# Kernel tuning notes

Measured on AMD Instinct MI355X. Metric: run time of the kernel, lower is better.

Reference implementation:

```python
import jax, jax.numpy as jnp
import numpy as np

N_TASKS = 32
D = 2097152  # flattened gradient dim
MAX_ITER = 250
STOP_CRIT = 1e-6
EPS = 1e-8


def setup_inputs() -> dict:
    key = jax.random.key(0)
    vecs = jax.random.normal(key, (N_TASKS, D), dtype=jnp.float32)
    return {"vecs": vecs}


def _line_solver(v11, v12, v22):
    # min-norm point on the segment between two vectors (vectorized / scalar)
    g = (v22 - v12) / (v11 + v22 - 2.0 * v12 + EPS)
    c = v22 + g * (v12 - v22)
    gamma = jnp.where(v12 >= v22, 0.0, g)
    gamma = jnp.where(v12 >= v11, 1.0, gamma)
    cost = jnp.where(v12 >= v22, v22, c)
    cost = jnp.where(v12 >= v11, v11, cost)
    return gamma, cost


def _planar_init(G, n):
    iu_np, ju_np = np.triu_indices(n, 1)
    iu = jnp.asarray(iu_np)
    ju = jnp.asarray(ju_np)
    vivj = G[iu, ju]
    vivi = G[iu, iu]
    vjvj = G[ju, ju]
    gamma, cost = _line_solver(vivi, vivj, vjvj)
    off = jnp.argmin(cost)
    sol = jnp.zeros(n, dtype=G.dtype)
    sol = sol.at[iu[off]].set(gamma[off]).at[ju[off]].set(1.0 - gamma[off])
    return sol


def _proj_simplex(gamma, i_grid):
    s = jnp.sort(gamma)[::-1]  # descending
    tmp_max = (jnp.cumsum(s) - 1.0) / i_grid
    cond = tmp_max[:-1] > s[1:]
    first = jnp.argmax(cond)  # index of first True (0 if none)
    tmax = jnp.where(jnp.any(cond), tmp_max[:-1][first], tmp_max[-1])
    return jnp.maximum(gamma - tmax, 0.0)


def _next_point(cur, grad, n, i_grid):
    proj = grad - jnp.sum(grad) / n
    neg = proj < 0
    pos = proj > 0
    tm1 = jnp.where(neg, -cur / jnp.where(neg, proj, 1.0), jnp.inf)
    tm2 = jnp.where(pos, (1.0 - cur) / jnp.where(pos, proj, 1.0), jnp.inf)
    m1 = jnp.min(jnp.where(tm1 > 1e-7, tm1, jnp.inf))
    t = jnp.where(jnp.isfinite(m1), m1, 1.0)
    m2 = jnp.min(jnp.where(tm2 > 1e-7, tm2, jnp.inf))
    t = jnp.minimum(t, m2)  # no-op if m2 is inf
    nxt = proj * t + cur
    return _proj_simplex(nxt, i_grid)


def reference(vecs):
    n = vecs.shape[0]
    G = vecs @ vecs.T  # [n, n] grammian; only memory-heavy step
    sol0 = _planar_init(G, n)
    i_grid = jnp.arange(n, dtype=G.dtype) + 1.0
    n_f = jnp.asarray(n, dtype=G.dtype)

    def body(carry, _):
        sol, done = carry
        grad_dir = -(G @ sol)
        newp = _next_point(sol, grad_dir, n_f, i_grid)
        Gs = G @ sol
        Gn = G @ newp
        v11 = sol @ Gs
        v12 = sol @ Gn
        v22 = newp @ Gn
        gamma, _ = _line_solver(v11, v12, v22)
        new_sol = gamma * sol + (1.0 - gamma) * newp
        stop = jnp.sum(jnp.abs(new_sol - sol)) < STOP_CRIT
        nd = done | stop
        # original returns the OLD sol_vec when change < stop_crit
        out = jnp.where(nd, sol, new_sol)
        return (out, nd), None

    (sol, _), _ = jax.lax.scan(body, (sol0, jnp.array(False)), None, length=MAX_ITER)
    return sol
```

## Files before the change

### kernel.cpp

```cpp
#include <hip/hip_runtime.h>

#define NT 32
#define EPSF 1e-8f

#define TILE_COLS 64
#define GR_THREADS 256
#define WAVES_PB 4
#define TILES_PW 8

__global__ __launch_bounds__(GR_THREADS, 1)
void gram_kernel(const float* __restrict__ vecs, double* __restrict__ Gd, int D)
{
    __shared__ __align__(16) float tile[WAVES_PB][TILE_COLS * 32];
    __shared__ float Gpart[NT * NT];

    const int tid  = threadIdx.x;
    const int wave = tid >> 6;
    const int lane = tid & 63;

    for (int e = tid; e < NT * NT; e += GR_THREADS) Gpart[e] = 0.0f;
    __syncthreads();

    float* my = tile[wave];
    const int swz = lane & 7;

    const int cj = lane >> 4;
    const int pi = (lane >> 2) & 3;
    const int pk = lane & 3;

    float acc[8][8];
#pragma unroll
    for (int r = 0; r < 8; r++)
#pragma unroll
        for (int c = 0; c < 8; c++) acc[r][c] = 0.0f;

    const unsigned base0 = (unsigned)blockIdx.x * (WAVES_PB * TILES_PW * TILE_COLS)
                         + (unsigned)wave * (TILES_PW * TILE_COLS) + (unsigned)lane;

    float pre[32];
#pragma unroll
    for (int r = 0; r < 32; r++)
        pre[r] = (vecs + (size_t)r * (size_t)D)[base0];

    for (int t = 0; t < TILES_PW; t++) {
#pragma unroll
        for (int g = 0; g < 8; g++) {
            float4 w = make_float4(pre[4 * g + 0], pre[4 * g + 1],
                                   pre[4 * g + 2], pre[4 * g + 3]);
            *(float4*)(my + lane * 32 + ((g ^ swz) << 2)) = w;
        }
        if (t + 1 < TILES_PW) {
            const unsigned off = base0 + (unsigned)(t + 1) * TILE_COLS;
#pragma unroll
            for (int r = 0; r < 32; r++)
                pre[r] = (vecs + (size_t)r * (size_t)D)[off];
        }
        asm volatile("" ::: "memory");
#pragma unroll
        for (int jt = 0; jt < 16; jt++) {
            const int j = (jt << 2) + cj;
            const float* col = my + j * 32;
            const int js = j & 7;
            const float4 a0 = *(const float4*)(col + (((2 * pi) ^ js) << 2));
            const float4 a1 = *(const float4*)(col + (((2 * pi + 1) ^ js) << 2));
            const float4 b0 = *(const float4*)(col + (((2 * pk) ^ js) << 2));
            const float4 b1 = *(const float4*)(col + (((2 * pk + 1) ^ js) << 2));
            const float a[8] = {a0.x, a0.y, a0.z, a0.w, a1.x, a1.y, a1.z, a1.w};
            const float b[8] = {b0.x, b0.y, b0.z, b0.w, b1.x, b1.y, b1.z, b1.w};
#pragma unroll
            for (int r = 0; r < 8; r++)
#pragma unroll
                for (int c = 0; c < 8; c++)
                    acc[r][c] = fmaf(a[r], b[c], acc[r][c]);
        }
    }

#pragma unroll
    for (int r = 0; r < 8; r++)
#pragma unroll
        for (int c = 0; c < 8; c++) {
            float v = acc[r][c];
            v += __shfl_xor(v, 16);
            v += __shfl_xor(v, 32);
            if (lane < 16)
                atomicAdd(&Gpart[(8 * pi + r) * NT + (8 * pk + c)], v);
        }
    __syncthreads();
    for (int e = tid; e < NT * NT; e += GR_THREADS)
        atomicAdd(&Gd[e], (double)Gpart[e]);
}

template<int CTRL>
__device__ __forceinline__ float dpp0(float x) {
    return __int_as_float(__builtin_amdgcn_update_dpp(
        0, __float_as_int(x), CTRL, 0xF, 0xF, true));
}
template<int CTRL>
__device__ __forceinline__ float dppk(float oldv, float x) {
    return __int_as_float(__builtin_amdgcn_update_dpp(
        __float_as_int(oldv), __float_as_int(x), CTRL, 0xF, 0xF, false));
}
__device__ __forceinline__ float rdlane(float x, int l) {
    return __int_as_float(__builtin_amdgcn_readlane(__float_as_int(x), l));
}

__device__ __forceinline__ float bsum32u(float v) {
    v += dpp0<0x111>(v);
    v += dpp0<0x112>(v);
    v += dpp0<0x114>(v);
    v += dpp0<0x118>(v);
    return rdlane(v, 15) + rdlane(v, 31);
}
__device__ __forceinline__ float bmin32u(float v) {
    v = fminf(v, dppk<0x111>(v, v));
    v = fminf(v, dppk<0x112>(v, v));
    v = fminf(v, dppk<0x114>(v, v));
    v = fminf(v, dppk<0x118>(v, v));
    return fminf(rdlane(v, 15), rdlane(v, 31));
}

__global__ __launch_bounds__(64)
void solver_kernel(const double* __restrict__ Gd, float* __restrict__ out)
{
    __shared__ float Gsh[NT * 33];
    __shared__ __align__(16) float xb0[64];
    __shared__ __align__(16) float xb1[64];
    __shared__ __align__(16) float xb2[64];

    const int lane = threadIdx.x;
    const int e = lane & 31;
    const int h = lane >> 5;

    for (int t2 = 0; t2 < 16; t2++) {
        int idx = t2 * 64 + lane;
        Gsh[(idx >> 5) * 33 + (idx & 31)] = (float)Gd[idx];
    }
    __syncthreads();

    float Grow[16];
#pragma unroll
    for (int k = 0; k < 16; k++)
        Grow[k] = Gsh[e * 33 + 16 * h + k];

    const int hb = h * 48;
    const float4* xr0 = (const float4*)(xb0 + hb);
    const float4* xr1 = (const float4*)(xb1 + hb);
    const float4* xr2 = (const float4*)(xb2 + hb);

    auto mv = [&](const float4* xr) -> float {
        const float4 q0 = xr[0], q1 = xr[1], q2 = xr[2], q3 = xr[3];
        const float xv[16] = {q0.x, q0.y, q0.z, q0.w, q1.x, q1.y, q1.z, q1.w,
                              q2.x, q2.y, q2.z, q2.w, q3.x, q3.y, q3.z, q3.w};
        float a0 = 0.0f, a1 = 0.0f;
#pragma unroll
        for (int s = 0; s < 16; s += 2) {
            a0 = fmaf(Grow[s + 0], xv[s + 0], a0);
            a1 = fmaf(Grow[s + 1], xv[s + 1], a1);
        }
        float half = a0 + a1;
        return half + __shfl_xor(half, 32);
    };

    float bestCost = INFINITY, bestGamma = 0.0f;
    int bestEnc = 0x7FFFFFFF;
    for (int a = 0; a < NT - 1; a++) {
        int b = a + 1 + lane;
        if (b < NT) {
            float v11 = Gsh[a * 33 + a];
            float v12 = Gsh[a * 33 + b];
            float v22 = Gsh[b * 33 + b];
            float g = (v22 - v12) / (v11 + v22 - 2.0f * v12 + EPSF);
            float c = v22 + g * (v12 - v22);
            float gamma = (v12 >= v22) ? 0.0f : g;
            float cost  = (v12 >= v22) ? v22 : c;
            if (v12 >= v11) { gamma = 1.0f; cost = v11; }
            int enc = a * NT + b;
            if (cost < bestCost) { bestCost = cost; bestEnc = enc; bestGamma = gamma; }
        }
    }
#pragma unroll
    for (int m = 1; m < 64; m <<= 1) {
        float oc = __shfl_xor(bestCost, m);
        int   oe = __shfl_xor(bestEnc, m);
        float og = __shfl_xor(bestGamma, m);
        if (oc < bestCost || (oc == bestCost && oe < bestEnc)) {
            bestCost = oc; bestEnc = oe; bestGamma = og;
        }
    }
    const int bi = bestEnc >> 5, bj = bestEnc & 31;

    float sol = 0.0f;
    if (e == bi) sol = bestGamma;
    if (e == bj) sol = 1.0f - bestGamma;

    xb0[lane] = sol;

    float GsolRec = 0.0f;

    for (int it = 0; it < 250; it++) {
        float Gsol = ((it & 3) == 0) ? mv(xr0) : GsolRec;

        float grad = -Gsol;
        float proj = grad - bsum32u(grad) * 0.03125f;

        float tm1 = (proj < 0.0f) ? (-sol / proj) : INFINITY;
        float tm2 = (proj > 0.0f) ? ((1.0f - sol) / proj) : INFINITY;
        float m1 = bmin32u((tm1 > 1e-7f) ? tm1 : INFINITY);
        float m2 = bmin32u((tm2 > 1e-7f) ? tm2 : INFINITY);
        float t = __builtin_isinf(m1) ? 1.0f : m1;
        t = fminf(t, m2);
        float nxt = fmaf(proj, t, sol);

        int nb = __float_as_int(nxt);
        unsigned u = (unsigned)nb ^ ((nb < 0) ? 0xFFFFFFFFu : 0x80000000u);

        xb1[lane] = nxt;
        const float4 r0 = xr1[0], r1 = xr1[1], r2 = xr1[2], r3 = xr1[3];
        const float xj16[16] = {r0.x, r0.y, r0.z, r0.w, r1.x, r1.y, r1.z, r1.w,
                                r2.x, r2.y, r2.z, r2.w, r3.x, r3.y, r3.z, r3.w};

        int rank = 0;
        float S = 0.0f;
        const int dtie = e - 16 * h;
#pragma unroll
        for (int s = 0; s < 16; s++) {
            float xj = xj16[s];
            int nbj = __float_as_int(xj);
            unsigned uj = (unsigned)nbj ^ ((nbj < 0) ? 0xFFFFFFFFu : 0x80000000u);
            bool gt = (uj > u) || ((uj == u) && (s < dtie));
            rank += gt ? 1 : 0;
            S += gt ? xj : 0.0f;
        }
        rank += __shfl_xor(rank, 32);
        S += __shfl_xor(S, 32);

        float total = bsum32u(nxt);

        float cand = (S - 1.0f) / (float)rank;
        bool cond = (rank >= 1) && (cand > nxt);
        float rmin = bmin32u(cond ? (float)rank : INFINITY);
        unsigned long long msk = __ballot(cond && ((float)rank == rmin));
        int src = (int)__ffsll(msk) - 1;
        float tmax = (msk == 0ull)
                   ? (total - 1.0f) * 0.03125f
                   : rdlane(cand, src);
        float newp = fmaxf(nxt - tmax, 0.0f);

        xb2[lane] = newp;
        float Gn = mv(xr2);

        float z = (h == 0) ? (sol * Gsol) : (newp * Gn);
        z += dpp0<0x111>(z);
        z += dpp0<0x112>(z);
        z += dpp0<0x114>(z);
        z += dpp0<0x118>(z);
        float v11 = rdlane(z, 15) + rdlane(z, 31);
        float v22 = rdlane(z, 47) + rdlane(z, 63);
        float v12 = bsum32u(sol * Gn);

        float g = (v22 - v12) / (v11 + v22 - 2.0f * v12 + EPSF);
        float gamma = (v12 >= v22) ? 0.0f : g;
        gamma = (v12 >= v11) ? 1.0f : gamma;

        float new_sol = gamma * sol + (1.0f - gamma) * newp;

        GsolRec = fmaf(gamma, Gsol, (1.0f - gamma) * Gn);

        float diff = bsum32u(fabsf(new_sol - sol));
        if (diff < 1e-6f) break;
        sol = new_sol;
        xb0[lane] = sol;
    }
    if (lane < NT) out[lane] = sol;
}

extern "C" void kernel_launch(void* const* d_in, const int* in_sizes, int n_in,
                              void* d_out, int out_size, void* d_ws, size_t ws_size,
                              hipStream_t stream) {
    const float* vecs = (const float*)d_in[0];
    float* out = (float*)d_out;
    double* Gd = (double*)d_ws;
    const int D = in_sizes[0] / NT;

    hipMemsetAsync(Gd, 0, NT * NT * sizeof(double), stream);

    const int cols_per_block = WAVES_PB * TILES_PW * TILE_COLS;
    const int grid = D / cols_per_block;
    gram_kernel<<<grid, GR_THREADS, 0, stream>>>(vecs, Gd, D);
    solver_kernel<<<1, 64, 0, stream>>>(Gd, out);
}
```

Before: 409.7 us.

## Replace global double atomics with per-block partials and a reduction kernel

Each gram block now writes its 32x32 partial Gram matrix to workspace instead of atomically adding doubles into a shared global matrix. A new reduce kernel sums the 1024 partials in double precision with wave shuffles and writes the final Gram matrix, which also removes the memset. This avoids contention on global fp64 atomics. In exchange it adds a kernel launch and a few MB of extra traffic, and it hardcodes 1024 partial blocks in the reduction.

```diff
diff --git a/kernel.cpp b/kernel.cpp
--- a/kernel.cpp
+++ b/kernel.cpp
@@ -9,7 +9,7 @@
 #define TILES_PW 8
 
 __global__ __launch_bounds__(GR_THREADS, 1)
-void gram_kernel(const float* __restrict__ vecs, double* __restrict__ Gd, int D)
+void gram_kernel(const float* __restrict__ vecs, float* __restrict__ part, int D)
 {
     __shared__ __align__(16) float tile[WAVES_PB][TILE_COLS * 32];
     __shared__ float Gpart[NT * NT];
@@ -86,8 +86,37 @@
                 atomicAdd(&Gpart[(8 * pi + r) * NT + (8 * pk + c)], v);
         }
     __syncthreads();
+    float* myPart = part + (size_t)blockIdx.x * (NT * NT);
     for (int e = tid; e < NT * NT; e += GR_THREADS)
-        atomicAdd(&Gd[e], (double)Gpart[e]);
+        myPart[e] = Gpart[e];
+}
+
+__global__ __launch_bounds__(64)
+void reduce_kernel(const float* __restrict__ part, double* __restrict__ Gd)
+{
+    const int g = blockIdx.x;
+    const int t = threadIdx.x;
+    double s0 = 0.0, s1 = 0.0, s2 = 0.0, s3 = 0.0;
+#pragma unroll
+    for (int j = 0; j < 16; j++) {
+        const float4 v = *(const float4*)(part
+            + (size_t)(t + 64 * j) * (NT * NT) + 4 * g);
+        s0 += (double)v.x; s1 += (double)v.y;
+        s2 += (double)v.z; s3 += (double)v.w;
+    }
+#pragma unroll
+    for (int m = 1; m < 64; m <<= 1) {
+        s0 += __shfl_xor(s0, m);
+        s1 += __shfl_xor(s1, m);
+        s2 += __shfl_xor(s2, m);
+        s3 += __shfl_xor(s3, m);
+    }
+    if (t == 0) {
+        Gd[4 * g + 0] = s0;
+        Gd[4 * g + 1] = s1;
+        Gd[4 * g + 2] = s2;
+        Gd[4 * g + 3] = s3;
+    }
 }
 
 template<int CTRL>
@@ -280,12 +309,13 @@
     const float* vecs = (const float*)d_in[0];
     float* out = (float*)d_out;
     double* Gd = (double*)d_ws;
+    float* part = (float*)((char*)d_ws + (1 << 20));
     const int D = in_sizes[0] / NT;
 
-    hipMemsetAsync(Gd, 0, NT * NT * sizeof(double), stream);
 
     const int cols_per_block = WAVES_PB * TILES_PW * TILE_COLS;
     const int grid = D / cols_per_block;
-    gram_kernel<<<grid, GR_THREADS, 0, stream>>>(vecs, Gd, D);
+    gram_kernel<<<grid, GR_THREADS, 0, stream>>>(vecs, part, D);
+    reduce_kernel<<<NT * NT / 4, 64, 0, stream>>>(part, Gd);
     solver_kernel<<<1, 64, 0, stream>>>(Gd, out);
 }
```

After: 414.2 us. Within noise of the previous version (+1.1%).
